# Performance work log

Measured on AMD Instinct MI355X. Metric: run time of the kernel, lower is better.

Reference implementation:

```python
import jax, jax.numpy as jnp
import numpy as np

T, B, H, IN = 256, 8, 128, 256  # passage_len, batch, hidden_size, input_size


def setup_inputs() -> dict:
    key = jax.random.key(0)
    ks = jax.random.split(key, 10)
    sc = 0.05
    return {
        "passage_repr": jax.random.normal(ks[0], (T, B, IN), jnp.float32),
        "passage_mask": jnp.ones((B, T), jnp.int32),  # unused by original forward
        "vT_w": jax.random.normal(ks[1], (1, H), jnp.float32) * sc,
        "WvP_w": jax.random.normal(ks[2], (H, IN), jnp.float32) * sc,
        "WvPbar_w": jax.random.normal(ks[3], (H, IN), jnp.float32) * sc,
        "gate_w": jax.random.normal(ks[4], (2 * H, 2 * H), jnp.float32) * sc,
        # GRU params: [layer(3), direction(2), ...]; all layers take 2H-dim input
        "gru_Wih": jax.random.normal(ks[5], (3, 2, 3 * H, 2 * H), jnp.float32) * sc,
        "gru_Whh": jax.random.normal(ks[6], (3, 2, 3 * H, H), jnp.float32) * sc,
        "gru_bih": jax.random.normal(ks[7], (3, 2, 3 * H), jnp.float32) * sc,
        "gru_bhh": jax.random.normal(ks[8], (3, 2, 3 * H), jnp.float32) * sc,
    }


def _gru_cell(x, h, Wih, Whh, bih, bhh):
    # PyTorch GRUCell math, gate order (r, z, n)
    gi = x @ Wih.T + bih
    gh = h @ Whh.T + bhh
    ir, iz, inn = jnp.split(gi, 3, axis=-1)
    hr, hz, hn = jnp.split(gh, 3, axis=-1)
    r = jax.nn.sigmoid(ir + hr)
    z = jax.nn.sigmoid(iz + hz)
    n = jnp.tanh(inn + r * hn)
    return (1.0 - z) * n + z * h


def reference(passage_repr, passage_mask, vT_w, WvP_w, WvPbar_w, gate_w,
              gru_Wih, gru_Whh, gru_bih, gru_bhh):
    t, b, _ = passage_repr.shape
    h = gru_Whh.shape[-1]

    prep = jnp.einsum('tbi,hi->tbh', passage_repr, WvP_w)     # WvP(passage_repr)
    pbar = jnp.einsum('tbi,hi->tbh', passage_repr, WvPbar_w)  # WvPbar(passage_repr)

    # Bahdanau scores: s[q,k,b] = vT . tanh(pbar[q] + prep[k]); softmax over k
    scores = jnp.einsum('qkbh,oh->qkb', jnp.tanh(pbar[:, None] + prep[None, :]), vT_w)
    a = jax.nn.softmax(scores, axis=1)                        # [Tq, Tk, B]
    ct = jnp.einsum('qkb,kbh->qbh', a, pbar)                  # values are pbar (as in source)

    u = jnp.concatenate([pbar, ct], axis=-1)                  # [T, B, 2H]
    u = u * jax.nn.sigmoid(jnp.einsum('tbd,ed->tbe', u, gate_w))

    def step(hstate, x):
        # hstate: [6, B, H]; layout prev[2l]=fwd, prev[2l+1]=bwd of layer l
        new_h = []
        layer_in = x
        for l in range(3):
            hf = _gru_cell(layer_in, hstate[2 * l], gru_Wih[l, 0], gru_Whh[l, 0], gru_bih[l, 0], gru_bhh[l, 0])
            hb = _gru_cell(layer_in, hstate[2 * l + 1], gru_Wih[l, 1], gru_Whh[l, 1], gru_bih[l, 1], gru_bhh[l, 1])
            new_h += [hf, hb]
            layer_in = jnp.concatenate([hf, hb], axis=-1)     # [B, 2H]
        return jnp.stack(new_h), layer_in

    h0 = jnp.zeros((6, b, h), passage_repr.dtype)
    _, result = jax.lax.scan(step, h0, u)                     # [T, B, 2H]
    return jnp.transpose(result, (1, 0, 2))                   # [B, T, 2H] (eval: no dropout)
```

## Files before the change

### kernel.cpp

```cpp
#include <hip/hip_runtime.h>
#include <hip/hip_bf16.h>

#define T_LEN 256
#define CHUNK 8
#define NCHUNK (T_LEN / CHUNK)

typedef _Float16 f16x8 __attribute__((ext_vector_type(8)));
typedef float f32x4 __attribute__((ext_vector_type(4)));

__device__ __forceinline__ float fsig(float x) {
  return __builtin_amdgcn_rcpf(1.f + __expf(-x));
}
__device__ __forceinline__ float ftanhf(float x) {
  return fmaf(-2.f, __builtin_amdgcn_rcpf(1.f + __expf(2.f * x)), 1.f);
}

#define MFMA16(a,b,c) __builtin_amdgcn_mfma_f32_16x16x32_f16(a, b, c, 0, 0, 0)
#define PIN(x) asm volatile("" : "+v"(*reinterpret_cast<f32x4*>(&(x))))

__global__ void k_prep(const float* __restrict__ WvP, const float* __restrict__ WvPb,
                       const float* __restrict__ gatew,
                       const float* __restrict__ Wih, const float* __restrict__ Whh,
                       float* __restrict__ WvPT, float* __restrict__ WvPbT,
                       float* __restrict__ gwT, float* __restrict__ Wih0T,
                       _Float16* __restrict__ Wx, _Float16* __restrict__ Wh,
                       unsigned* __restrict__ flags) {
  int n = blockIdx.x*blockDim.x + threadIdx.x;
  int NT = gridDim.x*blockDim.x;
  if (n < 128) flags[n] = 0u;
  for (int k = n; k < 256*128; k += NT) {
    int i = k >> 7, h = k & 127;
    WvPT[k]  = WvP[h*256 + i];
    WvPbT[k] = WvPb[h*256 + i];
  }
  for (int k = n; k < 256*256; k += NT) {
    int dd = k >> 8, e = k & 255;
    gwT[k] = gatew[e*256 + dd];
  }
  for (int k = n; k < 256*768; k += NT) {
    int i = k / 768, doo = k % 768;
    Wih0T[k] = Wih[(size_t)doo*256 + i];
  }
  for (int k = n; k < 6*384*128; k += NT) {
    Wh[k] = (_Float16)Whh[k];
  }
  for (int k = n; k < 4*384*256; k += NT) {
    Wx[k] = (_Float16)Wih[(size_t)2*384*256 + k];
  }
}

__global__ __launch_bounds__(256) void k_prep_pbar(
    const float* __restrict__ P, const float* __restrict__ WvPT,
    const float* __restrict__ WvPbT, float* __restrict__ prepT,
    float* __restrict__ pbar) {
  __shared__ float Pl[4*256];
  int R0 = blockIdx.x * 4, tid = threadIdx.x;
  for (int k = tid; k < 1024; k += 256) Pl[k] = P[(size_t)R0*256 + k];
  __syncthreads();
  int h = tid & 127;
  const float* Wt = (tid < 128) ? WvPT : WvPbT;
  float acc[4] = {0,0,0,0};
  for (int i = 0; i < 256; ++i) {
    float w = Wt[i*128 + h];
    acc[0] += Pl[i]*w; acc[1] += Pl[256+i]*w;
    acc[2] += Pl[512+i]*w; acc[3] += Pl[768+i]*w;
  }
  #pragma unroll
  for (int r = 0; r < 4; ++r) {
    int R = R0 + r, t = R >> 3, b = R & 7;
    if (tid < 128) prepT[((size_t)b*128 + h)*256 + t] = acc[r];
    else           pbar[(size_t)R*128 + h] = acc[r];
  }
}

__global__ __launch_bounds__(256) void k_attn(
    const float* __restrict__ prepT, const float* __restrict__ pbar,
    const float* __restrict__ vw, const float* __restrict__ gwT,
    float* __restrict__ ug) {
  int b = blockIdx.x & 7, q0 = (blockIdx.x >> 3) * 4;
  int tid = threadIdx.x;
  __shared__ float u[4][256];
  __shared__ float vl[128];
  __shared__ float sc[4][256];
  __shared__ float red[4];
  if (tid < 128) vl[tid] = vw[tid];
  for (int k = tid; k < 512; k += 256) {
    int j = k >> 7, h = k & 127;
    u[j][h] = pbar[(((size_t)(q0+j))*8 + b)*128 + h];
  }
  __syncthreads();
  float s[4] = {0,0,0,0};
  for (int h = 0; h < 128; ++h) {
    float pk = prepT[((size_t)b*128 + h)*256 + tid];
    float vh = vl[h];
    #pragma unroll
    for (int j = 0; j < 4; ++j) {
      float e = __expf(2.f*(u[j][h] + pk));
      float t = __builtin_amdgcn_rcpf(e + 1.f);
      s[j] = fmaf(vh, fmaf(-2.f, t, 1.f), s[j]);
    }
  }
  #pragma unroll
  for (int j = 0; j < 4; ++j) {
    float v = s[j];
    #pragma unroll
    for (int off = 32; off > 0; off >>= 1) v = fmaxf(v, __shfl_xor(v, off));
    if ((tid & 63) == 0) red[tid >> 6] = v;
    __syncthreads();
    float m = fmaxf(fmaxf(red[0], red[1]), fmaxf(red[2], red[3]));
    __syncthreads();
    float e = __expf(s[j] - m);
    v = e;
    #pragma unroll
    for (int off = 32; off > 0; off >>= 1) v += __shfl_xor(v, off);
    if ((tid & 63) == 0) red[tid >> 6] = v;
    __syncthreads();
    float sum = red[0] + red[1] + red[2] + red[3];
    __syncthreads();
    sc[j][tid] = e * __builtin_amdgcn_rcpf(sum);
  }
  __syncthreads();
  {
    int h = tid & 127, jj = tid >> 7;
    float c0 = 0.f, c1 = 0.f;
    for (int k = 0; k < 256; ++k) {
      float p = pbar[((size_t)k*8 + b)*128 + h];
      c0 += sc[jj][k]   * p;
      c1 += sc[jj+2][k] * p;
    }
    u[jj][128+h]   = c0;
    u[jj+2][128+h] = c1;
  }
  __syncthreads();
  {
    float gg[4] = {0,0,0,0};
    for (int dd = 0; dd < 256; ++dd) {
      float w = gwT[(size_t)dd*256 + tid];
      #pragma unroll
      for (int j = 0; j < 4; ++j) gg[j] += u[j][dd] * w;
    }
    #pragma unroll
    for (int j = 0; j < 4; ++j) {
      float ue = u[j][tid];
      ug[(((size_t)(q0+j))*8 + b)*256 + tid] = ue * fsig(gg[j]);
    }
  }
}

__global__ __launch_bounds__(256) void k_gi0(
    const float* __restrict__ ug, const float* __restrict__ Wih0T,
    const float* __restrict__ bih, const float* __restrict__ bhh,
    float* __restrict__ gi0) {
  __shared__ float ul[8][256];
  __shared__ float st[768*8];
  int t = blockIdx.x, tid = threadIdx.x;
  for (int k = tid; k < 2048; k += 256) ul[k >> 8][k & 255] = ug[(size_t)t*2048 + k];
  __syncthreads();
  float acc[3][8];
  #pragma unroll
  for (int a = 0; a < 3; ++a)
    #pragma unroll
    for (int r = 0; r < 8; ++r) acc[a][r] = 0.f;
  for (int i = 0; i < 256; ++i) {
    float w0 = Wih0T[(size_t)i*768 + tid];
    float w1 = Wih0T[(size_t)i*768 + 256 + tid];
    float w2 = Wih0T[(size_t)i*768 + 512 + tid];
    #pragma unroll
    for (int r = 0; r < 8; ++r) {
      float uu = ul[r][i];
      acc[0][r] += uu*w0; acc[1][r] += uu*w1; acc[2][r] += uu*w2;
    }
  }
  #pragma unroll
  for (int a = 0; a < 3; ++a) {
    int o = a*256 + tid;
    int og = (o >= 384) ? (o - 384) : o;
    float ba = bih[o] + ((og < 256) ? bhh[o] : 0.f);
    #pragma unroll
    for (int r = 0; r < 8; ++r) st[o*8 + r] = acc[a][r] + ba;
  }
  __syncthreads();
  #pragma unroll
  for (int j = 0; j < 6; ++j) {
    int idx = j*256 + tid;
    ((f32x4*)gi0)[(size_t)t*1536 + idx] = ((const f32x4*)st)[idx];
  }
}

__global__ __launch_bounds__(512, 1) void k_gru12(
    const _Float16* __restrict__ Wx, const _Float16* __restrict__ Wh,
    const float* __restrict__ gi0, float* __restrict__ gi1,
    float* __restrict__ gi2, const float* __restrict__ bih,
    const float* __restrict__ bhh, unsigned long long* Hbuf,
    float* __restrict__ out, unsigned* flags)
{
  const int wg = blockIdx.x;
  const int tid = threadIdx.x;
  const int w = tid >> 6, lane = tid & 63;
  const int lo = lane & 15, hi = lane >> 4;

  __shared__ char LDSU[36864];

  if (wg < 6) {
    const int c = wg, l = c >> 1, d = c & 1;
    _Float16* hlds = (_Float16*)(LDSU + 32768);
    char* SL = LDSU;

    { f16x8 z = {0,0,0,0,0,0,0,0};
      for (int p = tid; p < 256; p += 512) ((f16x8*)hlds)[p] = z; }

    f16x8 bh[3][4];
    #pragma unroll
    for (int nt = 0; nt < 3; ++nt) {
      int o = 16*(w + 8*nt) + lo;
      #pragma unroll
      for (int ks = 0; ks < 4; ++ks)
        bh[nt][ks] = *(const f16x8*)(Wh + ((size_t)c*384 + o)*128 + 32*ks + 8*hi);
    }
    #pragma unroll
    for (int nt = 0; nt < 3; ++nt)
      #pragma unroll
      for (int ks = 0; ks < 4; ++ks)
        PIN(bh[nt][ks]);

    const int hidx = 16*w + lo;
    const float b_hn = bhh[(size_t)c*384 + 256 + hidx];
    const int b0 = 4*(hi & 1);

    const float* gplain = gi0 + (size_t)d*384*8;
    const unsigned long long* gatom =
        (const unsigned long long*)((l == 1) ? gi1 : gi2) + (size_t)(d*384)*4;
    unsigned* fg = flags + 8 + (l > 0 ? (l-1)*32 : 0);

    f32x4 gA0,gA1,gA2, gB0,gB1,gB2;
    auto LD = [&](int t, f32x4& x0, f32x4& x1, f32x4& x2) {
      if (l == 0) {
        const float* g = gplain + (size_t)t*768*8;
        x0 = *(const f32x4*)(g + (size_t)hidx*8 + b0);
        x1 = *(const f32x4*)(g + ((size_t)128 + hidx)*8 + b0);
        x2 = *(const f32x4*)(g + ((size_t)256 + hidx)*8 + b0);
      } else {
        const unsigned long long* g = gatom + (size_t)t*3072 + (b0 >> 1);
        #pragma unroll
        for (int a = 0; a < 3; ++a) {
          size_t ix = (size_t)(a*128 + hidx)*4;
          unsigned long long u0 = __hip_atomic_load(g + ix,
              __ATOMIC_RELAXED, __HIP_MEMORY_SCOPE_AGENT);
          unsigned long long u1 = __hip_atomic_load(g + ix + 1,
              __ATOMIC_RELAXED, __HIP_MEMORY_SCOPE_AGENT);
          f32x4 v;
          ((unsigned long long*)&v)[0] = u0;
          ((unsigned long long*)&v)[1] = u1;
          if (a == 0) x0 = v; else if (a == 1) x1 = v; else x2 = v;
        }
      }
    };

    float hp[4] = {0,0,0,0};
    __syncthreads();

    for (int tc = 0; tc < NCHUNK; ++tc) {
      if (l > 0) {
        if (tid == 0) {
          while (__hip_atomic_load(fg + tc, __ATOMIC_RELAXED,
                                   __HIP_MEMORY_SCOPE_AGENT) == 0u)
            __builtin_amdgcn_s_sleep(2);
          __builtin_amdgcn_fence(__ATOMIC_ACQUIRE, "agent");
        }
        __syncthreads();
      }
      LD(tc*CHUNK, gA0, gA1, gA2);

      #pragma unroll
      for (int tt = 0; tt < CHUNK; ++tt) {
        const int t = tc*CHUNK + tt;
        f32x4 ax0, ax1, ax2;
        if (!(tt & 1)) {
          ax0 = gA0; ax1 = gA1; ax2 = gA2;
          if (tt < CHUNK-1 || (l == 0 && t < T_LEN-1)) LD(t+1, gB0, gB1, gB2);
        } else {
          ax0 = gB0; ax1 = gB1; ax2 = gB2;
          if (tt < CHUNK-1 || (l == 0 && t < T_LEN-1)) LD(t+1, gA0, gA1, gA2);
        }
        f32x4 ah0 = {0,0,0,0}, ah1 = {0,0,0,0}, ah2 = {0,0,0,0};
        {
          const char* hb = (const char*)hlds + (t & 1)*2048;
          f16x8 a[4];
          #pragma unroll
          for (int ks = 0; ks < 4; ++ks) {
            int byte = ((lo & 7)*256 + (32*ks + 8*hi)*2) ^ ((lo & 7) << 4);
            a[ks] = *(const f16x8*)(hb + byte);
          }
          #pragma unroll
          for (int ks = 0; ks < 4; ++ks) {
            ah0 = MFMA16(a[ks], bh[0][ks], ah0);
            ah1 = MFMA16(a[ks], bh[1][ks], ah1);
            ah2 = MFMA16(a[ks], bh[2][ks], ah2);
          }
        }
        float hn[4];
        #pragma unroll
        for (int q = 0; q < 4; ++q) {
          float r  = fsig(ax0[q] + ah0[q]);
          float z  = fsig(ax1[q] + ah1[q]);
          float nn = ftanhf(fmaf(r, ah2[q] + b_hn, ax2[q]));
          hn[q] = fmaf(z, hp[q] - nn, nn);
          hp[q] = hn[q];
        }
        if (lane < 32) {
          char* hb2 = (char*)hlds + ((t + 1) & 1)*2048;
          #pragma unroll
          for (int q = 0; q < 4; ++q) {
            int b = 4*hi + q;
            int byte = (b*256 + hidx*2) ^ (b << 4);
            *(_Float16*)(hb2 + byte) = (_Float16)hn[q];
            if (l < 2) *(_Float16*)(SL + (tt*8 + b)*256 + hidx*2) = (_Float16)hn[q];
            else       *(float*)   (SL + (tt*8 + b)*512 + hidx*4) = hn[q];
          }
        }
        asm volatile("s_waitcnt lgkmcnt(0)" ::: "memory");
        __builtin_amdgcn_s_barrier();
        __builtin_amdgcn_sched_barrier(0);
      }

      if (l < 2) {
        #pragma unroll
        for (int i = 0; i < 4; ++i) {
          int u = i*512 + tid;
          int tt2 = u >> 8, b = (u >> 5) & 7, pu = u & 31;
          unsigned long long v = *(const unsigned long long*)
              (SL + (tt2*8 + b)*256 + pu*8);
          __hip_atomic_store(Hbuf + (((size_t)c) << 16)
                                  + (size_t)(tc*CHUNK + tt2)*256 + b*32 + pu,
                             v, __ATOMIC_RELAXED, __HIP_MEMORY_SCOPE_AGENT);
        }
        asm volatile("s_waitcnt vmcnt(0)" ::: "memory");
        __syncthreads();
        if (tid == 0)
          __hip_atomic_store(flags + c, (unsigned)(tc + 1),
                             __ATOMIC_RELEASE, __HIP_MEMORY_SCOPE_AGENT);
      } else {
        #pragma unroll
        for (int i = 0; i < 4; ++i) {
          int u = i*512 + tid;
          int tt2 = u >> 8, b = (u >> 5) & 7, cc = u & 31;
          f32x4 v = *(const f32x4*)(SL + (tt2*8 + b)*512 + cc*16);
          *(f32x4*)(out + (((size_t)b*256 + tc*CHUNK + tt2)*256 + d*128 + cc*4)) = v;
        }
        asm volatile("s_waitcnt lgkmcnt(0)" ::: "memory");
        __builtin_amdgcn_s_barrier();
        __builtin_amdgcn_sched_barrier(0);
      }
    }
  } else {
    const int g  = wg - 6;
    const int lg = 1 + (g >> 4);
    const int cinf = (lg - 1) * 2;
    unsigned long long* gdst = (unsigned long long*)((lg == 1) ? gi1 : gi2);
    unsigned* fg = flags + 8 + (lg - 1)*32;
    _Float16* XL = (_Float16*)LDSU;

    for (int rep = 0; rep < 2; ++rep) {
      const int tc = (g & 15) + rep*16;
      const int t0 = tc * CHUNK;
      if (tid == 0) {
        while (__hip_atomic_load(flags + cinf, __ATOMIC_RELAXED,
                                 __HIP_MEMORY_SCOPE_AGENT) <= (unsigned)tc)
          __builtin_amdgcn_s_sleep(8);
        while (__hip_atomic_load(flags + cinf + 1, __ATOMIC_RELAXED,
                                 __HIP_MEMORY_SCOPE_AGENT) <= (unsigned)tc)
          __builtin_amdgcn_s_sleep(8);
        __builtin_amdgcn_fence(__ATOMIC_ACQUIRE, "agent");
      }
      __syncthreads();
      #pragma unroll
      for (int r = 0; r < 8; ++r) {
        int u = r*512 + tid;
        int cell = u >> 11, rem = u & 2047;
        int tt = rem >> 8, b = (rem >> 5) & 7, p = rem & 31;
        unsigned long long v = __hip_atomic_load(
            Hbuf + (((size_t)(cinf + cell)) << 16)
                 + (size_t)(t0 + tt)*256 + b*32 + p,
            __ATOMIC_RELAXED, __HIP_MEMORY_SCOPE_AGENT);
        int byte = (tt*4096 + b*512 + cell*256 + p*8) ^ ((b & 7) << 4);
        *(unsigned long long*)((char*)XL + byte) = v;
      }
      __syncthreads();

      f32x4 acc[2][3][4];
      #pragma unroll
      for (int c2 = 0; c2 < 2; ++c2)
        #pragma unroll
        for (int nt = 0; nt < 3; ++nt)
          #pragma unroll
          for (int mt = 0; mt < 4; ++mt) acc[c2][nt][mt] = (f32x4){0,0,0,0};

      for (int ks = 0; ks < 8; ++ks) {
        f16x8 a[4];
        #pragma unroll
        for (int mt = 0; mt < 4; ++mt) {
          int byte = ((mt*2 + (lo >> 3))*4096 + (lo & 7)*512 + 64*ks + 16*hi)
                     ^ ((lo & 7) << 4);
          a[mt] = *(const f16x8*)((const char*)XL + byte);
        }
        #pragma unroll
        for (int c2 = 0; c2 < 2; ++c2) {
          const size_t wb = (size_t)(2*lg + c2 - 2) * 384;
          #pragma unroll
          for (int nt = 0; nt < 3; ++nt) {
            f16x8 bw = *(const f16x8*)(Wx + (wb + 16*(w + 8*nt) + lo)*256
                                          + 32*ks + 8*hi);
            #pragma unroll
            for (int mt = 0; mt < 4; ++mt)
              acc[c2][nt][mt] = MFMA16(a[mt], bw, acc[c2][nt][mt]);
          }
        }
      }
      #pragma unroll
      for (int c2 = 0; c2 < 2; ++c2) {
        const int c = 2*lg + c2;
        #pragma unroll
        for (int nt = 0; nt < 3; ++nt) {
          int o = 16*(w + 8*nt) + lo;
          float badd = bih[(size_t)c*384 + o]
                     + ((o < 256) ? bhh[(size_t)c*384 + o] : 0.f);
          #pragma unroll
          for (int mt = 0; mt < 4; ++mt) {
            f32x4 v = acc[c2][nt][mt];
            v[0] += badd; v[1] += badd; v[2] += badd; v[3] += badd;
            int t = t0 + mt*2 + (hi >> 1), b0i = 4*(hi & 1);
            size_t ix = (size_t)t*3072 + (size_t)(c2*384 + o)*4 + (b0i >> 1);
            __hip_atomic_store(gdst + ix,     ((unsigned long long*)&v)[0],
                               __ATOMIC_RELAXED, __HIP_MEMORY_SCOPE_AGENT);
            __hip_atomic_store(gdst + ix + 1, ((unsigned long long*)&v)[1],
                               __ATOMIC_RELAXED, __HIP_MEMORY_SCOPE_AGENT);
          }
        }
      }
      asm volatile("s_waitcnt vmcnt(0)" ::: "memory");
      __syncthreads();
      if (tid == 0)
        __hip_atomic_store(fg + tc, 1u,
                           __ATOMIC_RELEASE, __HIP_MEMORY_SCOPE_AGENT);
      __syncthreads();
    }
  }
}

extern "C" void kernel_launch(void* const* d_in, const int* in_sizes, int n_in,
                              void* d_out, int out_size, void* d_ws, size_t ws_size,
                              hipStream_t stream) {
  (void)in_sizes; (void)n_in; (void)out_size; (void)ws_size;
  const float* P     = (const float*)d_in[0];
  const float* vw    = (const float*)d_in[2];
  const float* WvP   = (const float*)d_in[3];
  const float* WvPb  = (const float*)d_in[4];
  const float* gatew = (const float*)d_in[5];
  const float* Wih   = (const float*)d_in[6];
  const float* Whh   = (const float*)d_in[7];
  const float* bih   = (const float*)d_in[8];
  const float* bhh   = (const float*)d_in[9];
  float* out = (float*)d_out;

  char* wsp = (char*)d_ws;
  size_t off = 0;
  auto alloc = [&](size_t nbytes) -> void* {
    void* p = wsp + off;
    off += (nbytes + 255) & ~(size_t)255;
    return p;
  };
  float*    prepT = (float*)   alloc((size_t)8*128*256*4);
  float*    pbar  = (float*)   alloc((size_t)256*8*128*4);
  float*    ug    = (float*)   alloc((size_t)256*8*256*4);
  float*    gi0   = (float*)   alloc((size_t)256*768*8*4);
  float*    gi1   = (float*)   alloc((size_t)256*768*8*4);
  float*    gi2   = (float*)   alloc((size_t)256*768*8*4);
  unsigned long long* Hbuf = (unsigned long long*)alloc((size_t)4*256*8*32*8);
  _Float16* Wx    = (_Float16*)alloc((size_t)4*384*256*2);
  _Float16* Wh    = (_Float16*)alloc((size_t)6*384*128*2);
  float*    WvPT  = (float*)   alloc((size_t)256*128*4);
  float*    WvPbT = (float*)   alloc((size_t)256*128*4);
  float*    gwT   = (float*)   alloc((size_t)256*256*4);
  float*    Wih0T = (float*)   alloc((size_t)256*768*4);
  unsigned* flags = (unsigned*)alloc((size_t)128*4);

  hipLaunchKernelGGL(k_prep, dim3(256), dim3(256), 0, stream,
                     WvP, WvPb, gatew, Wih, Whh, WvPT, WvPbT, gwT, Wih0T, Wx, Wh,
                     flags);
  hipLaunchKernelGGL(k_prep_pbar, dim3(512), dim3(256), 0, stream,
                     P, WvPT, WvPbT, prepT, pbar);
  hipLaunchKernelGGL(k_attn, dim3(512), dim3(256), 0, stream,
                     prepT, pbar, vw, gwT, ug);
  hipLaunchKernelGGL(k_gi0, dim3(256), dim3(256), 0, stream,
                     ug, Wih0T, bih, bhh, gi0);
  hipLaunchKernelGGL(k_gru12, dim3(38), dim3(512), 0, stream,
                     Wx, Wh, gi0, gi1, gi2, bih, bhh, Hbuf, out, flags);
}
```

Measured before the change: 449.7 us.

## Fuse attention and layer-0 input projection into persistent GRU kernel with flag pipelining

Merges the attention kernel and the layer-0 input-gate GEMM into the persistent GRU kernel as extra workgroups. Attention blocks signal per-timestep-group counters, gi0 blocks wait on those and publish per-chunk flags, and layer-0 GRU workgroups consume chunks as they become ready. The aim is to overlap the recurrent scan with attention and projection work and to remove two kernel launch boundaries. It relies on all 198 workgroups being co-resident, since spin-waits on flags deadlock otherwise, and it splits the compute units between the attention work and the latency-bound recurrence.

After: 502.1 us (median of 2 runs). 1.12x slower.

```diff
diff --git a/kernel.cpp b/kernel.cpp
--- a/kernel.cpp
+++ b/kernel.cpp
@@ -27,7 +27,7 @@
                        unsigned* __restrict__ flags) {
   int n = blockIdx.x*blockDim.x + threadIdx.x;
   int NT = gridDim.x*blockDim.x;
-  if (n < 128) flags[n] = 0u;
+  if (n < 256) flags[n] = 0u;
   for (int k = n; k < 256*128; k += NT) {
     int i = k >> 7, h = k & 127;
     WvPT[k]  = WvP[h*256 + i];
@@ -73,126 +73,14 @@
   }
 }
 
-__global__ __launch_bounds__(256) void k_attn(
+__global__ __launch_bounds__(512, 1) void k_fused(
+    const _Float16* __restrict__ Wx, const _Float16* __restrict__ Wh,
     const float* __restrict__ prepT, const float* __restrict__ pbar,
     const float* __restrict__ vw, const float* __restrict__ gwT,
-    float* __restrict__ ug) {
-  int b = blockIdx.x & 7, q0 = (blockIdx.x >> 3) * 4;
-  int tid = threadIdx.x;
-  __shared__ float u[4][256];
-  __shared__ float vl[128];
-  __shared__ float sc[4][256];
-  __shared__ float red[4];
-  if (tid < 128) vl[tid] = vw[tid];
-  for (int k = tid; k < 512; k += 256) {
-    int j = k >> 7, h = k & 127;
-    u[j][h] = pbar[(((size_t)(q0+j))*8 + b)*128 + h];
-  }
-  __syncthreads();
-  float s[4] = {0,0,0,0};
-  for (int h = 0; h < 128; ++h) {
-    float pk = prepT[((size_t)b*128 + h)*256 + tid];
-    float vh = vl[h];
-    #pragma unroll
-    for (int j = 0; j < 4; ++j) {
-      float e = __expf(2.f*(u[j][h] + pk));
-      float t = __builtin_amdgcn_rcpf(e + 1.f);
-      s[j] = fmaf(vh, fmaf(-2.f, t, 1.f), s[j]);
-    }
-  }
-  #pragma unroll
-  for (int j = 0; j < 4; ++j) {
-    float v = s[j];
-    #pragma unroll
-    for (int off = 32; off > 0; off >>= 1) v = fmaxf(v, __shfl_xor(v, off));
-    if ((tid & 63) == 0) red[tid >> 6] = v;
-    __syncthreads();
-    float m = fmaxf(fmaxf(red[0], red[1]), fmaxf(red[2], red[3]));
-    __syncthreads();
-    float e = __expf(s[j] - m);
-    v = e;
-    #pragma unroll
-    for (int off = 32; off > 0; off >>= 1) v += __shfl_xor(v, off);
-    if ((tid & 63) == 0) red[tid >> 6] = v;
-    __syncthreads();
-    float sum = red[0] + red[1] + red[2] + red[3];
-    __syncthreads();
-    sc[j][tid] = e * __builtin_amdgcn_rcpf(sum);
-  }
-  __syncthreads();
-  {
-    int h = tid & 127, jj = tid >> 7;
-    float c0 = 0.f, c1 = 0.f;
-    for (int k = 0; k < 256; ++k) {
-      float p = pbar[((size_t)k*8 + b)*128 + h];
-      c0 += sc[jj][k]   * p;
-      c1 += sc[jj+2][k] * p;
-    }
-    u[jj][128+h]   = c0;
-    u[jj+2][128+h] = c1;
-  }
-  __syncthreads();
-  {
-    float gg[4] = {0,0,0,0};
-    for (int dd = 0; dd < 256; ++dd) {
-      float w = gwT[(size_t)dd*256 + tid];
-      #pragma unroll
-      for (int j = 0; j < 4; ++j) gg[j] += u[j][dd] * w;
-    }
-    #pragma unroll
-    for (int j = 0; j < 4; ++j) {
-      float ue = u[j][tid];
-      ug[(((size_t)(q0+j))*8 + b)*256 + tid] = ue * fsig(gg[j]);
-    }
-  }
-}
-
-__global__ __launch_bounds__(256) void k_gi0(
-    const float* __restrict__ ug, const float* __restrict__ Wih0T,
+    const float* __restrict__ Wih0T, float* __restrict__ ug,
+    float* __restrict__ gi0, float* __restrict__ gi1, float* __restrict__ gi2,
     const float* __restrict__ bih, const float* __restrict__ bhh,
-    float* __restrict__ gi0) {
-  __shared__ float ul[8][256];
-  __shared__ float st[768*8];
-  int t = blockIdx.x, tid = threadIdx.x;
-  for (int k = tid; k < 2048; k += 256) ul[k >> 8][k & 255] = ug[(size_t)t*2048 + k];
-  __syncthreads();
-  float acc[3][8];
-  #pragma unroll
-  for (int a = 0; a < 3; ++a)
-    #pragma unroll
-    for (int r = 0; r < 8; ++r) acc[a][r] = 0.f;
-  for (int i = 0; i < 256; ++i) {
-    float w0 = Wih0T[(size_t)i*768 + tid];
-    float w1 = Wih0T[(size_t)i*768 + 256 + tid];
-    float w2 = Wih0T[(size_t)i*768 + 512 + tid];
-    #pragma unroll
-    for (int r = 0; r < 8; ++r) {
-      float uu = ul[r][i];
-      acc[0][r] += uu*w0; acc[1][r] += uu*w1; acc[2][r] += uu*w2;
-    }
-  }
-  #pragma unroll
-  for (int a = 0; a < 3; ++a) {
-    int o = a*256 + tid;
-    int og = (o >= 384) ? (o - 384) : o;
-    float ba = bih[o] + ((og < 256) ? bhh[o] : 0.f);
-    #pragma unroll
-    for (int r = 0; r < 8; ++r) st[o*8 + r] = acc[a][r] + ba;
-  }
-  __syncthreads();
-  #pragma unroll
-  for (int j = 0; j < 6; ++j) {
-    int idx = j*256 + tid;
-    ((f32x4*)gi0)[(size_t)t*1536 + idx] = ((const f32x4*)st)[idx];
-  }
-}
-
-__global__ __launch_bounds__(512, 1) void k_gru12(
-    const _Float16* __restrict__ Wx, const _Float16* __restrict__ Wh,
-    const float* __restrict__ gi0, float* __restrict__ gi1,
-    float* __restrict__ gi2, const float* __restrict__ bih,
-    const float* __restrict__ bhh, unsigned long long* Hbuf,
-    float* __restrict__ out, unsigned* flags)
+    unsigned long long* Hbuf, float* __restrict__ out, unsigned* flags)
 {
   const int wg = blockIdx.x;
   const int tid = threadIdx.x;
@@ -227,32 +115,24 @@
     const float b_hn = bhh[(size_t)c*384 + 256 + hidx];
     const int b0 = 4*(hi & 1);
 
-    const float* gplain = gi0 + (size_t)d*384*8;
-    const unsigned long long* gatom =
-        (const unsigned long long*)((l == 1) ? gi1 : gi2) + (size_t)(d*384)*4;
+    const unsigned long long* gatom = (const unsigned long long*)
+        ((l == 0) ? gi0 : (l == 1) ? gi1 : gi2) + (size_t)(d*384)*4;
     unsigned* fg = flags + 8 + (l > 0 ? (l-1)*32 : 0);
 
     f32x4 gA0,gA1,gA2, gB0,gB1,gB2;
     auto LD = [&](int t, f32x4& x0, f32x4& x1, f32x4& x2) {
-      if (l == 0) {
-        const float* g = gplain + (size_t)t*768*8;
-        x0 = *(const f32x4*)(g + (size_t)hidx*8 + b0);
-        x1 = *(const f32x4*)(g + ((size_t)128 + hidx)*8 + b0);
-        x2 = *(const f32x4*)(g + ((size_t)256 + hidx)*8 + b0);
-      } else {
-        const unsigned long long* g = gatom + (size_t)t*3072 + (b0 >> 1);
-        #pragma unroll
-        for (int a = 0; a < 3; ++a) {
-          size_t ix = (size_t)(a*128 + hidx)*4;
-          unsigned long long u0 = __hip_atomic_load(g + ix,
-              __ATOMIC_RELAXED, __HIP_MEMORY_SCOPE_AGENT);
-          unsigned long long u1 = __hip_atomic_load(g + ix + 1,
-              __ATOMIC_RELAXED, __HIP_MEMORY_SCOPE_AGENT);
-          f32x4 v;
-          ((unsigned long long*)&v)[0] = u0;
-          ((unsigned long long*)&v)[1] = u1;
-          if (a == 0) x0 = v; else if (a == 1) x1 = v; else x2 = v;
-        }
+      const unsigned long long* g = gatom + (size_t)t*3072 + (b0 >> 1);
+      #pragma unroll
+      for (int a = 0; a < 3; ++a) {
+        size_t ix = (size_t)(a*128 + hidx)*4;
+        unsigned long long u0 = __hip_atomic_load(g + ix,
+            __ATOMIC_RELAXED, __HIP_MEMORY_SCOPE_AGENT);
+        unsigned long long u1 = __hip_atomic_load(g + ix + 1,
+            __ATOMIC_RELAXED, __HIP_MEMORY_SCOPE_AGENT);
+        f32x4 v;
+        ((unsigned long long*)&v)[0] = u0;
+        ((unsigned long long*)&v)[1] = u1;
+        if (a == 0) x0 = v; else if (a == 1) x1 = v; else x2 = v;
       }
     };
 
@@ -260,16 +140,21 @@
     __syncthreads();
 
     for (int tc = 0; tc < NCHUNK; ++tc) {
-      if (l > 0) {
-        if (tid == 0) {
+      if (tid == 0) {
+        if (l == 0) {
+          while (__hip_atomic_load(flags + 72 + tc, __ATOMIC_RELAXED,
+                                   __HIP_MEMORY_SCOPE_AGENT) == 0u)
+            __builtin_amdgcn_s_sleep(2);
+        } else {
           while (__hip_atomic_load(fg + tc, __ATOMIC_RELAXED,
                                    __HIP_MEMORY_SCOPE_AGENT) == 0u)
             __builtin_amdgcn_s_sleep(2);
-          __builtin_amdgcn_fence(__ATOMIC_ACQUIRE, "agent");
-        }
-        __syncthreads();
-      }
-      LD(tc*CHUNK, gA0, gA1, gA2);
+        }
+        __builtin_amdgcn_fence(__ATOMIC_ACQUIRE, "agent");
+      }
+      __syncthreads();
+      LD(tc*CHUNK,     gA0, gA1, gA2);
+      LD(tc*CHUNK + 1, gB0, gB1, gB2);
 
       #pragma unroll
       for (int tt = 0; tt < CHUNK; ++tt) {
@@ -277,10 +162,10 @@
         f32x4 ax0, ax1, ax2;
         if (!(tt & 1)) {
           ax0 = gA0; ax1 = gA1; ax2 = gA2;
-          if (tt < CHUNK-1 || (l == 0 && t < T_LEN-1)) LD(t+1, gB0, gB1, gB2);
+          if (tt + 2 < CHUNK) LD(t + 2, gA0, gA1, gA2);
         } else {
           ax0 = gB0; ax1 = gB1; ax2 = gB2;
-          if (tt < CHUNK-1 || (l == 0 && t < T_LEN-1)) LD(t+1, gA0, gA1, gA2);
+          if (tt + 2 < CHUNK) LD(t + 2, gB0, gB1, gB2);
         }
         f32x4 ah0 = {0,0,0,0}, ah1 = {0,0,0,0}, ah2 = {0,0,0,0};
         {
@@ -352,7 +237,7 @@
         __builtin_amdgcn_sched_barrier(0);
       }
     }
-  } else {
+  } else if (wg < 38) {
     const int g  = wg - 6;
     const int lg = 1 + (g >> 4);
     const int cinf = (lg - 1) * 2;
@@ -444,6 +329,140 @@
                            __ATOMIC_RELEASE, __HIP_MEMORY_SCOPE_AGENT);
       __syncthreads();
     }
+  } else if (wg < 166) {
+    float* u2   = (float*)LDSU;
+    float* sc2  = (float*)(LDSU + 8192);
+    float* vl   = (float*)(LDSU + 16384);
+    float* red2 = (float*)(LDSU + 16896);
+    const int side = tid >> 8, t2 = tid & 255;
+    float* uu = u2  + side*1024;
+    float* ss = sc2 + side*1024;
+    float* rr = red2 + side*4;
+
+    for (int rnd = 0; rnd < 2; ++rnd) {
+      const int inst = rnd*256 + (wg - 38)*2 + side;
+      const int b = inst & 7, q0 = (inst >> 3) << 2;
+      if (tid < 128) vl[tid] = vw[tid];
+      for (int k = t2; k < 512; k += 256) {
+        int j = k >> 7, h = k & 127;
+        uu[j*256 + h] = pbar[(((size_t)(q0+j))*8 + b)*128 + h];
+      }
+      __syncthreads();
+      float s[4] = {0,0,0,0};
+      for (int h = 0; h < 128; ++h) {
+        float pk = prepT[((size_t)b*128 + h)*256 + t2];
+        float vh = vl[h];
+        #pragma unroll
+        for (int j = 0; j < 4; ++j) {
+          float e = __expf(2.f*(uu[j*256 + h] + pk));
+          float tq = __builtin_amdgcn_rcpf(e + 1.f);
+          s[j] = fmaf(vh, fmaf(-2.f, tq, 1.f), s[j]);
+        }
+      }
+      #pragma unroll
+      for (int j = 0; j < 4; ++j) {
+        float v = s[j];
+        #pragma unroll
+        for (int off = 32; off > 0; off >>= 1) v = fmaxf(v, __shfl_xor(v, off));
+        if ((t2 & 63) == 0) rr[t2 >> 6] = v;
+        __syncthreads();
+        float m = fmaxf(fmaxf(rr[0], rr[1]), fmaxf(rr[2], rr[3]));
+        __syncthreads();
+        float e = __expf(s[j] - m);
+        v = e;
+        #pragma unroll
+        for (int off = 32; off > 0; off >>= 1) v += __shfl_xor(v, off);
+        if ((t2 & 63) == 0) rr[t2 >> 6] = v;
+        __syncthreads();
+        float sum = rr[0] + rr[1] + rr[2] + rr[3];
+        __syncthreads();
+        ss[j*256 + t2] = e * __builtin_amdgcn_rcpf(sum);
+      }
+      __syncthreads();
+      {
+        int h = t2 & 127, jj = t2 >> 7;
+        float c0 = 0.f, c1 = 0.f;
+        for (int k = 0; k < 256; ++k) {
+          float p = pbar[((size_t)k*8 + b)*128 + h];
+          c0 += ss[jj*256 + k]     * p;
+          c1 += ss[(jj+2)*256 + k] * p;
+        }
+        uu[jj*256 + 128 + h]     = c0;
+        uu[(jj+2)*256 + 128 + h] = c1;
+      }
+      __syncthreads();
+      {
+        float gg[4] = {0,0,0,0};
+        for (int dd = 0; dd < 256; ++dd) {
+          float wv = gwT[(size_t)dd*256 + t2];
+          #pragma unroll
+          for (int j = 0; j < 4; ++j) gg[j] += uu[j*256 + dd] * wv;
+        }
+        #pragma unroll
+        for (int j = 0; j < 4; ++j) {
+          float ue = uu[j*256 + t2];
+          ug[(((size_t)(q0+j))*8 + b)*256 + t2] = ue * fsig(gg[j]);
+        }
+      }
+      asm volatile("s_waitcnt vmcnt(0)" ::: "memory");
+      __syncthreads();
+      if (t2 == 0)
+        __hip_atomic_fetch_add(flags + 104 + (inst >> 3), 1u,
+                               __ATOMIC_RELEASE, __HIP_MEMORY_SCOPE_AGENT);
+      __syncthreads();
+    }
+  } else {
+    const int tc = wg - 166;
+    float* ul = (float*)LDSU;
+    const int side = tid >> 8, t2 = tid & 255;
+    float* us = ul + side*2048;
+    if (tid == 0) {
+      while (__hip_atomic_load(flags + 104 + 2*tc, __ATOMIC_RELAXED,
+                               __HIP_MEMORY_SCOPE_AGENT) < 8u)
+        __builtin_amdgcn_s_sleep(4);
+      while (__hip_atomic_load(flags + 104 + 2*tc + 1, __ATOMIC_RELAXED,
+                               __HIP_MEMORY_SCOPE_AGENT) < 8u)
+        __builtin_amdgcn_s_sleep(4);
+      __builtin_amdgcn_fence(__ATOMIC_ACQUIRE, "agent");
+    }
+    __syncthreads();
+    for (int tp = 0; tp < 4; ++tp) {
+      const int t = tc*8 + tp*2 + side;
+      for (int k = t2; k < 2048; k += 256)
+        us[(k >> 8)*256 + (k & 255)] = ug[(size_t)t*2048 + k];
+      __syncthreads();
+      float acc[3][8];
+      #pragma unroll
+      for (int a = 0; a < 3; ++a)
+        #pragma unroll
+        for (int r = 0; r < 8; ++r) acc[a][r] = 0.f;
+      for (int i = 0; i < 256; ++i) {
+        float w0 = Wih0T[(size_t)i*768 + t2];
+        float w1 = Wih0T[(size_t)i*768 + 256 + t2];
+        float w2 = Wih0T[(size_t)i*768 + 512 + t2];
+        #pragma unroll
+        for (int r = 0; r < 8; ++r) {
+          float uv = us[r*256 + i];
+          acc[0][r] += uv*w0; acc[1][r] += uv*w1; acc[2][r] += uv*w2;
+        }
+      }
+      #pragma unroll
+      for (int a = 0; a < 3; ++a) {
+        int o = a*256 + t2;
+        int og = (o >= 384) ? (o - 384) : o;
+        float ba = bih[o] + ((og < 256) ? bhh[o] : 0.f);
+        f32x4 v0 = {acc[a][0]+ba, acc[a][1]+ba, acc[a][2]+ba, acc[a][3]+ba};
+        f32x4 v1 = {acc[a][4]+ba, acc[a][5]+ba, acc[a][6]+ba, acc[a][7]+ba};
+        *(f32x4*)(gi0 + (size_t)t*6144 + o*8)     = v0;
+        *(f32x4*)(gi0 + (size_t)t*6144 + o*8 + 4) = v1;
+      }
+      __syncthreads();
+    }
+    asm volatile("s_waitcnt vmcnt(0)" ::: "memory");
+    __syncthreads();
+    if (tid == 0)
+      __hip_atomic_store(flags + 72 + tc, 1u,
+                         __ATOMIC_RELEASE, __HIP_MEMORY_SCOPE_AGENT);
   }
 }
 
@@ -482,17 +501,14 @@
   float*    WvPbT = (float*)   alloc((size_t)256*128*4);
   float*    gwT   = (float*)   alloc((size_t)256*256*4);
   float*    Wih0T = (float*)   alloc((size_t)256*768*4);
-  unsigned* flags = (unsigned*)alloc((size_t)128*4);
+  unsigned* flags = (unsigned*)alloc((size_t)256*4);
 
   hipLaunchKernelGGL(k_prep, dim3(256), dim3(256), 0, stream,
                      WvP, WvPb, gatew, Wih, Whh, WvPT, WvPbT, gwT, Wih0T, Wx, Wh,
                      flags);
   hipLaunchKernelGGL(k_prep_pbar, dim3(512), dim3(256), 0, stream,
                      P, WvPT, WvPbT, prepT, pbar);
-  hipLaunchKernelGGL(k_attn, dim3(512), dim3(256), 0, stream,
-                     prepT, pbar, vw, gwT, ug);
-  hipLaunchKernelGGL(k_gi0, dim3(256), dim3(256), 0, stream,
-                     ug, Wih0T, bih, bhh, gi0);
-  hipLaunchKernelGGL(k_gru12, dim3(38), dim3(512), 0, stream,
-                     Wx, Wh, gi0, gi1, gi2, bih, bhh, Hbuf, out, flags);
+  hipLaunchKernelGGL(k_fused, dim3(198), dim3(512), 0, stream,
+                     Wx, Wh, prepT, pbar, vw, gwT, Wih0T, ug,
+                     gi0, gi1, gi2, bih, bhh, Hbuf, out, flags);
 }
```

## Deepen gate-input prefetch, split MFMA accumulation chains, write last-layer output directly

Applied to the files above, without the earlier changes.

The recurrent GRU loop now prefetches input-gate values two timesteps ahead instead of one, and layer 0 primes the pipeline once before the chunk loop. The hidden-state MFMA reduction is split into two independent accumulator chains that are summed at the end, shortening the dependent MFMA latency on the serial critical path. The last layer writes each hidden value straight to global output instead of staging a chunk in LDS and flushing it behind an extra barrier. This uses more registers and issues scattered scalar global stores from the serial loop.

Measured after the change: 453.9 us, median of 2. No clear change (+0.9%).

```diff
diff --git a/kernel.cpp b/kernel.cpp
--- a/kernel.cpp
+++ b/kernel.cpp
@@ -187,7 +187,7 @@
   }
 }
 
-__global__ __launch_bounds__(512, 1) void k_gru12(
+__global__ __launch_bounds__(512, 1) void k_gru16(
     const _Float16* __restrict__ Wx, const _Float16* __restrict__ Wh,
     const float* __restrict__ gi0, float* __restrict__ gi1,
     float* __restrict__ gi2, const float* __restrict__ bih,
@@ -259,6 +259,11 @@
     float hp[4] = {0,0,0,0};
     __syncthreads();
 
+    if (l == 0) {
+      LD(0, gA0, gA1, gA2);
+      LD(1, gB0, gB1, gB2);
+    }
+
     for (int tc = 0; tc < NCHUNK; ++tc) {
       if (l > 0) {
         if (tid == 0) {
@@ -268,21 +273,24 @@
           __builtin_amdgcn_fence(__ATOMIC_ACQUIRE, "agent");
         }
         __syncthreads();
-      }
-      LD(tc*CHUNK, gA0, gA1, gA2);
+        LD(tc*CHUNK,     gA0, gA1, gA2);
+        LD(tc*CHUNK + 1, gB0, gB1, gB2);
+      }
 
       #pragma unroll
       for (int tt = 0; tt < CHUNK; ++tt) {
         const int t = tc*CHUNK + tt;
         f32x4 ax0, ax1, ax2;
+        const bool more = (tt + 2 < CHUNK) || (l == 0 && t + 2 < T_LEN);
         if (!(tt & 1)) {
           ax0 = gA0; ax1 = gA1; ax2 = gA2;
-          if (tt < CHUNK-1 || (l == 0 && t < T_LEN-1)) LD(t+1, gB0, gB1, gB2);
+          if (more) LD(t + 2, gA0, gA1, gA2);
         } else {
           ax0 = gB0; ax1 = gB1; ax2 = gB2;
-          if (tt < CHUNK-1 || (l == 0 && t < T_LEN-1)) LD(t+1, gA0, gA1, gA2);
+          if (more) LD(t + 2, gB0, gB1, gB2);
         }
         f32x4 ah0 = {0,0,0,0}, ah1 = {0,0,0,0}, ah2 = {0,0,0,0};
+        f32x4 bh0 = {0,0,0,0}, bh1 = {0,0,0,0}, bh2 = {0,0,0,0};
         {
           const char* hb = (const char*)hlds + (t & 1)*2048;
           f16x8 a[4];
@@ -291,12 +299,19 @@
             int byte = ((lo & 7)*256 + (32*ks + 8*hi)*2) ^ ((lo & 7) << 4);
             a[ks] = *(const f16x8*)(hb + byte);
           }
-          #pragma unroll
-          for (int ks = 0; ks < 4; ++ks) {
-            ah0 = MFMA16(a[ks], bh[0][ks], ah0);
-            ah1 = MFMA16(a[ks], bh[1][ks], ah1);
-            ah2 = MFMA16(a[ks], bh[2][ks], ah2);
-          }
+          ah0 = MFMA16(a[0], bh[0][0], ah0);
+          ah1 = MFMA16(a[0], bh[1][0], ah1);
+          ah2 = MFMA16(a[0], bh[2][0], ah2);
+          bh0 = MFMA16(a[2], bh[0][2], bh0);
+          bh1 = MFMA16(a[2], bh[1][2], bh1);
+          bh2 = MFMA16(a[2], bh[2][2], bh2);
+          ah0 = MFMA16(a[1], bh[0][1], ah0);
+          ah1 = MFMA16(a[1], bh[1][1], ah1);
+          ah2 = MFMA16(a[1], bh[2][1], ah2);
+          bh0 = MFMA16(a[3], bh[0][3], bh0);
+          bh1 = MFMA16(a[3], bh[1][3], bh1);
+          bh2 = MFMA16(a[3], bh[2][3], bh2);
+          ah0 += bh0; ah1 += bh1; ah2 += bh2;
         }
         float hn[4];
         #pragma unroll
@@ -315,7 +330,7 @@
             int byte = (b*256 + hidx*2) ^ (b << 4);
             *(_Float16*)(hb2 + byte) = (_Float16)hn[q];
             if (l < 2) *(_Float16*)(SL + (tt*8 + b)*256 + hidx*2) = (_Float16)hn[q];
-            else       *(float*)   (SL + (tt*8 + b)*512 + hidx*4) = hn[q];
+            else       out[((size_t)b*256 + t)*256 + d*128 + hidx] = hn[q];
           }
         }
         asm volatile("s_waitcnt lgkmcnt(0)" ::: "memory");
@@ -339,17 +354,6 @@
         if (tid == 0)
           __hip_atomic_store(flags + c, (unsigned)(tc + 1),
                              __ATOMIC_RELEASE, __HIP_MEMORY_SCOPE_AGENT);
-      } else {
-        #pragma unroll
-        for (int i = 0; i < 4; ++i) {
-          int u = i*512 + tid;
-          int tt2 = u >> 8, b = (u >> 5) & 7, cc = u & 31;
-          f32x4 v = *(const f32x4*)(SL + (tt2*8 + b)*512 + cc*16);
-          *(f32x4*)(out + (((size_t)b*256 + tc*CHUNK + tt2)*256 + d*128 + cc*4)) = v;
-        }
-        asm volatile("s_waitcnt lgkmcnt(0)" ::: "memory");
-        __builtin_amdgcn_s_barrier();
-        __builtin_amdgcn_sched_barrier(0);
       }
     }
   } else {
@@ -493,6 +497,6 @@
                      prepT, pbar, vw, gwT, ug);
   hipLaunchKernelGGL(k_gi0, dim3(256), dim3(256), 0, stream,
                      ug, Wih0T, bih, bhh, gi0);
-  hipLaunchKernelGGL(k_gru12, dim3(38), dim3(512), 0, stream,
+  hipLaunchKernelGGL(k_gru16, dim3(38), dim3(512), 0, stream,
                      Wx, Wh, gi0, gi1, gi2, bih, bhh, Hbuf, out, flags);
 }
```
